# Kernel optimization log

Measured on AMD Instinct MI355X. Metric: run time of the kernel, lower is better.

## Reference

```python
import jax, jax.numpy as jnp
import numpy as np

NEG = jnp.float32(-1e30)  # finite stand-in for -inf in masked max
SLOPE = 0.01              # F.leaky_relu default negative slope


def _lrelu(v):
    return jnp.where(v >= 0, v, SLOPE * v)


def _mlp(pts, w1, b1, w2, b2, w3, b3):
    # pts: [2, N] -> [64, N]; 1x1 Conv1d == pointwise linear over channel dim
    z = _lrelu(w1 @ pts + b1[:, None])
    z = _lrelu(w2 @ z + b2[:, None])
    z = _lrelu(w3 @ z + b3[:, None])
    return z


def setup_inputs() -> dict:
    key = jax.random.key(0)
    ks = jax.random.split(key, 10)
    B, C, H, W = 4, 19, 256, 256
    x = jax.random.randint(ks[0], (B, C, H, W), 0, 2, dtype=jnp.int32)
    # grid exactly as in the torch module: meshgrid of two linspaces, flattened
    g = np.array(np.meshgrid(np.linspace(-1, 1, 256), np.linspace(-1, 1, 256),
                             sparse=False)).astype(np.float32)  # [2,256,256]
    grid = jnp.asarray(g.reshape(2, -1))  # [2, 65536]
    w1 = jax.random.normal(ks[1], (64, 2), jnp.float32) * 0.5
    b1 = jax.random.normal(ks[2], (64,), jnp.float32) * 0.1
    w2 = jax.random.normal(ks[3], (64, 64), jnp.float32) * 0.125
    b2 = jax.random.normal(ks[4], (64,), jnp.float32) * 0.1
    w3 = jax.random.normal(ks[5], (64, 64), jnp.float32) * 0.125
    b3 = jax.random.normal(ks[6], (64,), jnp.float32) * 0.1
    fcw = jax.random.normal(ks[7], (512, 64 * C), jnp.float32)
    fcb = jax.random.normal(ks[8], (512,), jnp.float32) * 0.1
    return {"x": x, "grid": grid, "w1": w1, "b1": b1, "w2": w2, "b2": b2,
            "w3": w3, "b3": b3, "fcw": fcw, "fcb": fcb}


def reference(x, grid, w1, b1, w2, b2, w3, b3, fcw, fcb):
    B, C = x.shape[0], x.shape[1]
    # Pointwise MLP on the shared grid once (grid identical for all b,c)
    feats = _mlp(grid, w1, b1, w2, b2, w3, b3)                 # [64, N]
    # Fallback feature for empty masks: MLP on a single zero point
    zero_feat = _mlp(jnp.zeros((2, 1), feats.dtype),
                     w1, b1, w2, b2, w3, b3)[:, 0]             # [64]
    mask = (x.reshape(B, C, -1) == 1)                          # [B, C, N]
    # Masked max over the ragged point sets, fully vectorized
    masked = jnp.where(mask[:, :, None, :], feats[None, None], NEG)
    z = jnp.max(masked, axis=-1)                               # [B, C, 64]
    empty = ~jnp.any(mask, axis=-1)                            # [B, C]
    z = jnp.where(empty[..., None], zero_feat, z)
    flat = z.reshape(B, C * 64)                                # channel-major cat
    # EqualLinear: weight scaled by 1/sqrt(in_dim) (lr_mul=1)
    scale = jnp.float32(1.0 / np.sqrt(C * 64))
    out = flat @ (fcw * scale).T + fcb                         # [B, 512]
    return jnp.repeat(out[:, None, :], 18, axis=1)             # [B, 18, 512]
```

## Files before the change

### kernel.cpp

```cpp
#include <hip/hip_runtime.h>

#define NPTS  65536
#define NBC   76
#define NREP  8
#define KEYN  4864

typedef _Float16 f16;
typedef __fp16   h16x2 __attribute__((ext_vector_type(2)));
typedef _Float16 f16x8 __attribute__((ext_vector_type(8)));
typedef float    f32x4 __attribute__((ext_vector_type(4)));

__device__ __forceinline__ float lrelu(float v) { return fmaxf(v, 0.01f * v); }

__device__ __forceinline__ unsigned pkrtz(float lo, float hi) {
  h16x2 p = __builtin_amdgcn_cvt_pkrtz(lo, hi);
  return __builtin_bit_cast(unsigned, p);
}
__device__ __forceinline__ unsigned pkey(unsigned u) {
  unsigned t = (u >> 15) & 0x00010001u;
  return u ^ (0x80008000u | (t * 0x7FFFu));
}
__device__ __forceinline__ unsigned pkmax(unsigned a, unsigned b) {
  unsigned d;
  asm("v_pk_max_u16 %0, %1, %2" : "=v"(d) : "v"(a), "v"(b));
  return d;
}
__device__ __forceinline__ unsigned sext1(unsigned x, int b) {
  return (unsigned)(((int)(x << (31 - b))) >> 31);
}

__device__ __forceinline__ void mfma_layer(
    const f16* __restrict__ A, const f16* __restrict__ B,
    const float* __restrict__ bias,
    int chb, int c15, int q, int pt0, int pt1,
    f32x4& acc0, f32x4& acc1)
{
  float4 bv = *(const float4*)(bias + chb + q * 4);
  acc0 = (f32x4){bv.x, bv.y, bv.z, bv.w};
  acc1 = acc0;
  #pragma unroll
  for (int k0 = 0; k0 < 64; k0 += 32) {
    f16x8 af = *(const f16x8*)&A[(chb + c15) * 72 + k0 + q * 8];
    f16x8 b0 = *(const f16x8*)&B[pt0 * 72 + k0 + q * 8];
    f16x8 b1 = *(const f16x8*)&B[pt1 * 72 + k0 + q * 8];
    acc0 = __builtin_amdgcn_mfma_f32_16x16x32_f16(af, b0, acc0, 0, 0, 0);
    acc1 = __builtin_amdgcn_mfma_f32_16x16x32_f16(af, b1, acc1, 0, 0, 0);
  }
}

__device__ __forceinline__ void layer1(
    f16* __restrict__ zA, const float* __restrict__ w1,
    const float* __restrict__ b1, int wv, int lane, float g0, float g1)
{
  unsigned uo[4];
  #pragma unroll
  for (int p = 0; p < 4; ++p) {
    int j = wv * 8 + p * 2;
    float z0 = lrelu(w1[2 * j] * g0 + w1[2 * j + 1] * g1 + b1[j]);
    float z1 = lrelu(w1[2 * j + 2] * g0 + w1[2 * j + 3] * g1 + b1[j + 1]);
    uo[p] = pkrtz(z0, z1);
  }
  *(uint4*)&zA[lane * 72 + wv * 8] = make_uint4(uo[0], uo[1], uo[2], uo[3]);
}

__global__ __launch_bounds__(512, 4) void kA_mlp(
    const float* __restrict__ grid,
    const float* __restrict__ w1, const float* __restrict__ b1,
    const float* __restrict__ w2, const float* __restrict__ b2,
    const float* __restrict__ w3, const float* __restrict__ b3,
    unsigned* __restrict__ kbuf)
{
  __shared__ __align__(16) unsigned char smem[55296];
  f16* zA0 = (f16*)(smem);
  f16* zA1 = (f16*)(smem + 9216);
  f16* zB0 = (f16*)(smem + 18432);
  f16* zB1 = (f16*)(smem + 27648);
  f16* wf2 = (f16*)(smem + 36864);
  f16* wf3 = (f16*)(smem + 46080);

  const int t = threadIdx.x, lane = t & 63, wv = t >> 6;
  const int n0 = blockIdx.x * 128;

  float g0a = grid[n0 + lane],      g1a = grid[NPTS + n0 + lane];
  float g0b = grid[n0 + 64 + lane], g1b = grid[NPTS + n0 + 64 + lane];

  {
    int ch = t >> 3, k0 = (t & 7) * 8;
    const float4* s2 = (const float4*)(w2 + ch * 64 + k0);
    float4 a = s2[0], b = s2[1];
    *(uint4*)&wf2[ch * 72 + k0] =
        make_uint4(pkrtz(a.x, a.y), pkrtz(a.z, a.w), pkrtz(b.x, b.y), pkrtz(b.z, b.w));
    const float4* s3 = (const float4*)(w3 + ch * 64 + k0);
    float4 c = s3[0], d = s3[1];
    *(uint4*)&wf3[ch * 72 + k0] =
        make_uint4(pkrtz(c.x, c.y), pkrtz(c.z, c.w), pkrtz(d.x, d.y), pkrtz(d.z, d.w));
  }
  layer1(zA0, w1, b1, wv, lane, g0a, g1a);
  __syncthreads();

  const int chb = (wv & 3) * 16, pth = (wv >> 2) * 32;
  const int c15 = lane & 15, q = lane >> 4;
  const int chq = chb + q * 4;
  const int pt0 = pth + c15, pt1 = pth + 16 + c15;
  const int r0 = chq >> 1;

  {
    f32x4 a0, a1;
    mfma_layer(wf2, zA0, b2, chb, c15, q, pt0, pt1, a0, a1);
    *(uint2*)&zB0[pt0 * 72 + chq] =
        make_uint2(pkrtz(lrelu(a0[0]), lrelu(a0[1])), pkrtz(lrelu(a0[2]), lrelu(a0[3])));
    *(uint2*)&zB0[pt1 * 72 + chq] =
        make_uint2(pkrtz(lrelu(a1[0]), lrelu(a1[1])), pkrtz(lrelu(a1[2]), lrelu(a1[3])));
  }
  layer1(zA1, w1, b1, wv, lane, g0b, g1b);
  __syncthreads();

  {
    f32x4 c0, c1;
    mfma_layer(wf3, zB0, b3, chb, c15, q, pt0, pt1, c0, c1);
    unsigned* kb = kbuf + (unsigned)(blockIdx.x * 2) * 2048;
    kb[r0 * 64 + pt0]       = pkey(pkrtz(lrelu(c0[0]), lrelu(c0[1])));
    kb[(r0 + 1) * 64 + pt0] = pkey(pkrtz(lrelu(c0[2]), lrelu(c0[3])));
    kb[r0 * 64 + pt1]       = pkey(pkrtz(lrelu(c1[0]), lrelu(c1[1])));
    kb[(r0 + 1) * 64 + pt1] = pkey(pkrtz(lrelu(c1[2]), lrelu(c1[3])));
  }
  {
    f32x4 a0, a1;
    mfma_layer(wf2, zA1, b2, chb, c15, q, pt0, pt1, a0, a1);
    *(uint2*)&zB1[pt0 * 72 + chq] =
        make_uint2(pkrtz(lrelu(a0[0]), lrelu(a0[1])), pkrtz(lrelu(a0[2]), lrelu(a0[3])));
    *(uint2*)&zB1[pt1 * 72 + chq] =
        make_uint2(pkrtz(lrelu(a1[0]), lrelu(a1[1])), pkrtz(lrelu(a1[2]), lrelu(a1[3])));
  }
  __syncthreads();

  {
    f32x4 c0, c1;
    mfma_layer(wf3, zB1, b3, chb, c15, q, pt0, pt1, c0, c1);
    unsigned* kb = kbuf + (unsigned)(blockIdx.x * 2 + 1) * 2048;
    kb[r0 * 64 + pt0]       = pkey(pkrtz(lrelu(c0[0]), lrelu(c0[1])));
    kb[(r0 + 1) * 64 + pt0] = pkey(pkrtz(lrelu(c0[2]), lrelu(c0[3])));
    kb[r0 * 64 + pt1]       = pkey(pkrtz(lrelu(c1[0]), lrelu(c1[1])));
    kb[(r0 + 1) * 64 + pt1] = pkey(pkrtz(lrelu(c1[2]), lrelu(c1[3])));
  }
}

__device__ __forceinline__ void phaseB(
    const unsigned* __restrict__ zk, const unsigned* mlo, const unsigned* mhi,
    unsigned* uacc, int rw)
{
  #pragma unroll
  for (int np = 0; np < 16; ++np) {
    uint4 z4 = *(const uint4*)&zk[rw * 68 + np * 4];
    const int p = np * 4, pb = p & 31;
    #pragma unroll
    for (int ii = 0; ii < 5; ++ii) {
      unsigned m = (p < 32) ? mlo[ii] : mhi[ii];
      unsigned s0 = sext1(m, pb),     s1 = sext1(m, pb + 1);
      unsigned s2 = sext1(m, pb + 2), s3 = sext1(m, pb + 3);
      unsigned a = uacc[ii];
      a = pkmax(a, z4.x & s0); a = pkmax(a, z4.y & s1);
      a = pkmax(a, z4.z & s2); a = pkmax(a, z4.w & s3);
      uacc[ii] = a;
    }
  }
}

__global__ __launch_bounds__(512, 8) void kB_max(
    const int* __restrict__ x, const unsigned* __restrict__ kbuf,
    unsigned* __restrict__ keys)
{
  __shared__ unsigned zk0[32 * 68], zk1[32 * 68];
  __shared__ unsigned long long mb0[NBC], mb1[NBC];

  const int t = threadIdx.x, lane = t & 63, wv = t >> 6;
  const int n0 = blockIdx.x * 128;

  uint4 kv0 = *(const uint4*)(kbuf + (unsigned)(blockIdx.x * 2) * 2048 + t * 4);
  uint4 kv1 = *(const uint4*)(kbuf + (unsigned)(blockIdx.x * 2 + 1) * 2048 + t * 4);

  *(uint4*)&zk0[(t >> 4) * 68 + (t & 15) * 4] = kv0;

  {
    int xa[10];
    #pragma unroll
    for (int i = 0; i < 10; ++i) {
      int bc = wv + 8 * i;
      if (bc < NBC) xa[i] = x[(bc << 16) + n0 + lane];
    }
    #pragma unroll
    for (int i = 0; i < 10; ++i) {
      int bc = wv + 8 * i;
      if (bc < NBC) {
        unsigned long long m = __ballot(xa[i] == 1);
        if (lane == 0) mb0[bc] = m;
      }
    }
    #pragma unroll
    for (int i = 0; i < 10; ++i) {
      int bc = wv + 8 * i;
      if (bc < NBC) xa[i] = x[(bc << 16) + n0 + 64 + lane];
    }
    #pragma unroll
    for (int i = 0; i < 10; ++i) {
      int bc = wv + 8 * i;
      if (bc < NBC) {
        unsigned long long m = __ballot(xa[i] == 1);
        if (lane == 0) mb1[bc] = m;
      }
    }
  }
  __syncthreads();
  *(uint4*)&zk1[(t >> 4) * 68 + (t & 15) * 4] = kv1;

  const int rw = t & 31, bg = t >> 5;
  const int bc0 = bg * 5;

  unsigned uacc[5] = {0u, 0u, 0u, 0u, 0u};
  unsigned mlo[5], mhi[5];

  #pragma unroll
  for (int ii = 0; ii < 5; ++ii) {
    int bc = bc0 + ii;
    unsigned long long m = (bc < NBC) ? mb0[bc] : 0ull;
    mlo[ii] = (unsigned)m; mhi[ii] = (unsigned)(m >> 32);
  }
  phaseB(zk0, mlo, mhi, uacc, rw);
  __syncthreads();
  #pragma unroll
  for (int ii = 0; ii < 5; ++ii) {
    int bc = bc0 + ii;
    unsigned long long m = (bc < NBC) ? mb1[bc] : 0ull;
    mlo[ii] = (unsigned)m; mhi[ii] = (unsigned)(m >> 32);
  }
  phaseB(zk1, mlo, mhi, uacc, rw);

  unsigned* krep = keys + (blockIdx.x & (NREP - 1)) * KEYN;
  #pragma unroll
  for (int ii = 0; ii < 5; ++ii) {
    int bc = bc0 + ii;
    if (bc < NBC) {
      unsigned lo = uacc[ii] & 0xFFFFu, hi = uacc[ii] >> 16;
      if (lo) atomicMax(&krep[bc * 64 + 2 * rw], lo);
      if (hi) atomicMax(&krep[bc * 64 + 2 * rw + 1], hi);
    }
  }
}

__global__ __launch_bounds__(256) void k2_fc(
    const unsigned* __restrict__ keys,
    const float* __restrict__ b1, const float* __restrict__ w2,
    const float* __restrict__ b2, const float* __restrict__ w3,
    const float* __restrict__ b3,
    const float* __restrict__ fcw, const float* __restrict__ fcb,
    float* __restrict__ out)
{
  __shared__ float flat[4864];
  __shared__ float za[64], zb[64], zf[64];
  const int t = threadIdx.x;

  if (t < 64) za[t] = lrelu(b1[t]);
  __syncthreads();
  if (t < 64) {
    float s = b2[t];
    #pragma unroll 8
    for (int k = 0; k < 64; ++k) s += w2[t * 64 + k] * za[k];
    zb[t] = lrelu(s);
  }
  __syncthreads();
  if (t < 64) {
    float s = b3[t];
    #pragma unroll 8
    for (int k = 0; k < 64; ++k) s += w3[t * 64 + k] * zb[k];
    zf[t] = lrelu(s);
  }
  __syncthreads();

  for (int idx = t; idx < 4864; idx += 256) {
    unsigned m = keys[idx];
    #pragma unroll
    for (int r = 1; r < NREP; ++r) m = max(m, keys[r * KEYN + idx]);
    float v;
    if (m) {
      unsigned u = (m & 0x8000u) ? (m ^ 0x8000u) : (~m & 0xFFFFu);
      unsigned short us = (unsigned short)u;
      v = (float)__builtin_bit_cast(f16, us);
    } else {
      v = zf[idx & 63];
    }
    flat[idx] = v;
  }
  __syncthreads();

  const int wv = t >> 6, lane = t & 63;
  const int o = blockIdx.x * 4 + wv;
  const float* wrow = fcw + o * 1216;
  float fa0 = 0.f, fa1 = 0.f, fa2 = 0.f, fa3 = 0.f;
  #pragma unroll
  for (int i = 0; i < 19; ++i) {
    int jj = i * 64 + lane;
    float wvv = wrow[jj];
    fa0 += wvv * flat[jj];
    fa1 += wvv * flat[1216 + jj];
    fa2 += wvv * flat[2432 + jj];
    fa3 += wvv * flat[3648 + jj];
  }
  #pragma unroll
  for (int off = 32; off > 0; off >>= 1) {
    fa0 += __shfl_xor(fa0, off);
    fa1 += __shfl_xor(fa1, off);
    fa2 += __shfl_xor(fa2, off);
    fa3 += __shfl_xor(fa3, off);
  }
  const float scale = 0.028676966733820225f;
  float cb = fcb[o];
  if (lane < 18) {
    out[(0 * 18 + lane) * 512 + o] = fa0 * scale + cb;
    out[(1 * 18 + lane) * 512 + o] = fa1 * scale + cb;
    out[(2 * 18 + lane) * 512 + o] = fa2 * scale + cb;
    out[(3 * 18 + lane) * 512 + o] = fa3 * scale + cb;
  }
}

extern "C" void kernel_launch(void* const* d_in, const int* in_sizes, int n_in,
                              void* d_out, int out_size, void* d_ws, size_t ws_size,
                              hipStream_t stream)
{
  const int*   x    = (const int*)d_in[0];
  const float* grid = (const float*)d_in[1];
  const float* w1   = (const float*)d_in[2];
  const float* b1   = (const float*)d_in[3];
  const float* w2   = (const float*)d_in[4];
  const float* b2   = (const float*)d_in[5];
  const float* w3   = (const float*)d_in[6];
  const float* b3   = (const float*)d_in[7];
  const float* fcw  = (const float*)d_in[8];
  const float* fcb  = (const float*)d_in[9];
  float* out = (float*)d_out;

  unsigned* keys = (unsigned*)d_ws;
  unsigned* kbuf = (unsigned*)d_ws + 65536;

  (void)hipMemsetAsync(d_ws, 0, NREP * KEYN * sizeof(unsigned), stream);
  hipLaunchKernelGGL(kA_mlp, dim3(512), dim3(512), 0, stream,
                     grid, w1, b1, w2, b2, w3, b3, kbuf);
  hipLaunchKernelGGL(kB_max, dim3(512), dim3(512), 0, stream,
                     x, kbuf, keys);
  hipLaunchKernelGGL(k2_fc, dim3(128), dim3(256), 0, stream,
                     keys, b1, w2, b2, w3, b3, fcw, fcb, out);
}
```

Baseline: 126.7 us.

## Fold key zeroing into MLP kernel and keep fp16 weights in registers

Removes the separate hipMemsetAsync by having the first 76 blocks of the MLP kernel zero the key buffer (76*512 = NREP*KEYN entries). Layer-2/3 weight fragments are now loaded from global and converted straight into registers instead of staged in shared memory, which cuts LDS use from 55 KB to 36 KB. Launch bounds are raised to 8 blocks per CU, and the layer-1 and layer-2 work is reordered so both point halves run between fewer barriers. The cost is redundant per-wave global weight loads and more register pressure under the tighter occupancy bound.

```diff
diff --git a/kernel.cpp b/kernel.cpp
--- a/kernel.cpp
+++ b/kernel.cpp
@@ -28,23 +28,27 @@
 __device__ __forceinline__ unsigned sext1(unsigned x, int b) {
   return (unsigned)(((int)(x << (31 - b))) >> 31);
 }
-
-__device__ __forceinline__ void mfma_layer(
-    const f16* __restrict__ A, const f16* __restrict__ B,
-    const float* __restrict__ bias,
-    int chb, int c15, int q, int pt0, int pt1,
-    f32x4& acc0, f32x4& acc1)
-{
-  float4 bv = *(const float4*)(bias + chb + q * 4);
+__device__ __forceinline__ f16x8 ldcvt8(const float* p) {
+  float4 a = *(const float4*)p, b = *(const float4*)(p + 4);
+  uint4 u = make_uint4(pkrtz(a.x, a.y), pkrtz(a.z, a.w),
+                       pkrtz(b.x, b.y), pkrtz(b.z, b.w));
+  return __builtin_bit_cast(f16x8, u);
+}
+
+__device__ __forceinline__ void mfma_layer_r(
+    const f16x8* wr, const f16* __restrict__ B, const float* __restrict__ bias,
+    int chq, int q, int pt0, int pt1, f32x4& acc0, f32x4& acc1)
+{
+  float4 bv = *(const float4*)(bias + chq);
   acc0 = (f32x4){bv.x, bv.y, bv.z, bv.w};
   acc1 = acc0;
   #pragma unroll
-  for (int k0 = 0; k0 < 64; k0 += 32) {
-    f16x8 af = *(const f16x8*)&A[(chb + c15) * 72 + k0 + q * 8];
+  for (int s = 0; s < 2; ++s) {
+    int k0 = s * 32;
     f16x8 b0 = *(const f16x8*)&B[pt0 * 72 + k0 + q * 8];
     f16x8 b1 = *(const f16x8*)&B[pt1 * 72 + k0 + q * 8];
-    acc0 = __builtin_amdgcn_mfma_f32_16x16x32_f16(af, b0, acc0, 0, 0, 0);
-    acc1 = __builtin_amdgcn_mfma_f32_16x16x32_f16(af, b1, acc1, 0, 0, 0);
+    acc0 = __builtin_amdgcn_mfma_f32_16x16x32_f16(wr[s], b0, acc0, 0, 0, 0);
+    acc1 = __builtin_amdgcn_mfma_f32_16x16x32_f16(wr[s], b1, acc1, 0, 0, 0);
   }
 }
 
@@ -63,40 +67,26 @@
   *(uint4*)&zA[lane * 72 + wv * 8] = make_uint4(uo[0], uo[1], uo[2], uo[3]);
 }
 
-__global__ __launch_bounds__(512, 4) void kA_mlp(
+__global__ __launch_bounds__(512, 8) void kA_mlp(
     const float* __restrict__ grid,
     const float* __restrict__ w1, const float* __restrict__ b1,
     const float* __restrict__ w2, const float* __restrict__ b2,
     const float* __restrict__ w3, const float* __restrict__ b3,
-    unsigned* __restrict__ kbuf)
-{
-  __shared__ __align__(16) unsigned char smem[55296];
+    unsigned* __restrict__ kbuf, unsigned* __restrict__ keys)
+{
+  __shared__ __align__(16) unsigned char smem[36864];
   f16* zA0 = (f16*)(smem);
   f16* zA1 = (f16*)(smem + 9216);
   f16* zB0 = (f16*)(smem + 18432);
   f16* zB1 = (f16*)(smem + 27648);
-  f16* wf2 = (f16*)(smem + 36864);
-  f16* wf3 = (f16*)(smem + 46080);
 
   const int t = threadIdx.x, lane = t & 63, wv = t >> 6;
   const int n0 = blockIdx.x * 128;
 
+  if (blockIdx.x < 76) keys[blockIdx.x * 512 + t] = 0u;
+
   float g0a = grid[n0 + lane],      g1a = grid[NPTS + n0 + lane];
   float g0b = grid[n0 + 64 + lane], g1b = grid[NPTS + n0 + 64 + lane];
-
-  {
-    int ch = t >> 3, k0 = (t & 7) * 8;
-    const float4* s2 = (const float4*)(w2 + ch * 64 + k0);
-    float4 a = s2[0], b = s2[1];
-    *(uint4*)&wf2[ch * 72 + k0] =
-        make_uint4(pkrtz(a.x, a.y), pkrtz(a.z, a.w), pkrtz(b.x, b.y), pkrtz(b.z, b.w));
-    const float4* s3 = (const float4*)(w3 + ch * 64 + k0);
-    float4 c = s3[0], d = s3[1];
-    *(uint4*)&wf3[ch * 72 + k0] =
-        make_uint4(pkrtz(c.x, c.y), pkrtz(c.z, c.w), pkrtz(d.x, d.y), pkrtz(d.z, d.w));
-  }
-  layer1(zA0, w1, b1, wv, lane, g0a, g1a);
-  __syncthreads();
 
   const int chb = (wv & 3) * 16, pth = (wv >> 2) * 32;
   const int c15 = lane & 15, q = lane >> 4;
@@ -104,44 +94,45 @@
   const int pt0 = pth + c15, pt1 = pth + 16 + c15;
   const int r0 = chq >> 1;
 
+  f16x8 wr2[2], wr3[2];
   {
-    f32x4 a0, a1;
-    mfma_layer(wf2, zA0, b2, chb, c15, q, pt0, pt1, a0, a1);
-    *(uint2*)&zB0[pt0 * 72 + chq] =
-        make_uint2(pkrtz(lrelu(a0[0]), lrelu(a0[1])), pkrtz(lrelu(a0[2]), lrelu(a0[3])));
-    *(uint2*)&zB0[pt1 * 72 + chq] =
-        make_uint2(pkrtz(lrelu(a1[0]), lrelu(a1[1])), pkrtz(lrelu(a1[2]), lrelu(a1[3])));
-  }
+    const int row = (chb + c15) * 64 + q * 8;
+    wr2[0] = ldcvt8(w2 + row);  wr2[1] = ldcvt8(w2 + row + 32);
+    wr3[0] = ldcvt8(w3 + row);  wr3[1] = ldcvt8(w3 + row + 32);
+  }
+
+  layer1(zA0, w1, b1, wv, lane, g0a, g1a);
   layer1(zA1, w1, b1, wv, lane, g0b, g1b);
   __syncthreads();
 
+  f32x4 a0, a1;
+  mfma_layer_r(wr2, zA0, b2, chq, q, pt0, pt1, a0, a1);
+  *(uint2*)&zB0[pt0 * 72 + chq] =
+      make_uint2(pkrtz(lrelu(a0[0]), lrelu(a0[1])), pkrtz(lrelu(a0[2]), lrelu(a0[3])));
+  *(uint2*)&zB0[pt1 * 72 + chq] =
+      make_uint2(pkrtz(lrelu(a1[0]), lrelu(a1[1])), pkrtz(lrelu(a1[2]), lrelu(a1[3])));
+  mfma_layer_r(wr2, zA1, b2, chq, q, pt0, pt1, a0, a1);
+  *(uint2*)&zB1[pt0 * 72 + chq] =
+      make_uint2(pkrtz(lrelu(a0[0]), lrelu(a0[1])), pkrtz(lrelu(a0[2]), lrelu(a0[3])));
+  *(uint2*)&zB1[pt1 * 72 + chq] =
+      make_uint2(pkrtz(lrelu(a1[0]), lrelu(a1[1])), pkrtz(lrelu(a1[2]), lrelu(a1[3])));
+  __syncthreads();
+
+  mfma_layer_r(wr3, zB0, b3, chq, q, pt0, pt1, a0, a1);
   {
-    f32x4 c0, c1;
-    mfma_layer(wf3, zB0, b3, chb, c15, q, pt0, pt1, c0, c1);
     unsigned* kb = kbuf + (unsigned)(blockIdx.x * 2) * 2048;
-    kb[r0 * 64 + pt0]       = pkey(pkrtz(lrelu(c0[0]), lrelu(c0[1])));
-    kb[(r0 + 1) * 64 + pt0] = pkey(pkrtz(lrelu(c0[2]), lrelu(c0[3])));
-    kb[r0 * 64 + pt1]       = pkey(pkrtz(lrelu(c1[0]), lrelu(c1[1])));
-    kb[(r0 + 1) * 64 + pt1] = pkey(pkrtz(lrelu(c1[2]), lrelu(c1[3])));
-  }
+    kb[r0 * 64 + pt0]       = pkey(pkrtz(lrelu(a0[0]), lrelu(a0[1])));
+    kb[(r0 + 1) * 64 + pt0] = pkey(pkrtz(lrelu(a0[2]), lrelu(a0[3])));
+    kb[r0 * 64 + pt1]       = pkey(pkrtz(lrelu(a1[0]), lrelu(a1[1])));
+    kb[(r0 + 1) * 64 + pt1] = pkey(pkrtz(lrelu(a1[2]), lrelu(a1[3])));
+  }
+  mfma_layer_r(wr3, zB1, b3, chq, q, pt0, pt1, a0, a1);
   {
-    f32x4 a0, a1;
-    mfma_layer(wf2, zA1, b2, chb, c15, q, pt0, pt1, a0, a1);
-    *(uint2*)&zB1[pt0 * 72 + chq] =
-        make_uint2(pkrtz(lrelu(a0[0]), lrelu(a0[1])), pkrtz(lrelu(a0[2]), lrelu(a0[3])));
-    *(uint2*)&zB1[pt1 * 72 + chq] =
-        make_uint2(pkrtz(lrelu(a1[0]), lrelu(a1[1])), pkrtz(lrelu(a1[2]), lrelu(a1[3])));
-  }
-  __syncthreads();
-
-  {
-    f32x4 c0, c1;
-    mfma_layer(wf3, zB1, b3, chb, c15, q, pt0, pt1, c0, c1);
     unsigned* kb = kbuf + (unsigned)(blockIdx.x * 2 + 1) * 2048;
-    kb[r0 * 64 + pt0]       = pkey(pkrtz(lrelu(c0[0]), lrelu(c0[1])));
-    kb[(r0 + 1) * 64 + pt0] = pkey(pkrtz(lrelu(c0[2]), lrelu(c0[3])));
-    kb[r0 * 64 + pt1]       = pkey(pkrtz(lrelu(c1[0]), lrelu(c1[1])));
-    kb[(r0 + 1) * 64 + pt1] = pkey(pkrtz(lrelu(c1[2]), lrelu(c1[3])));
+    kb[r0 * 64 + pt0]       = pkey(pkrtz(lrelu(a0[0]), lrelu(a0[1])));
+    kb[(r0 + 1) * 64 + pt0] = pkey(pkrtz(lrelu(a0[2]), lrelu(a0[3])));
+    kb[r0 * 64 + pt1]       = pkey(pkrtz(lrelu(a1[0]), lrelu(a1[1])));
+    kb[(r0 + 1) * 64 + pt1] = pkey(pkrtz(lrelu(a1[2]), lrelu(a1[3])));
   }
 }
 
@@ -178,7 +169,6 @@
 
   uint4 kv0 = *(const uint4*)(kbuf + (unsigned)(blockIdx.x * 2) * 2048 + t * 4);
   uint4 kv1 = *(const uint4*)(kbuf + (unsigned)(blockIdx.x * 2 + 1) * 2048 + t * 4);
-
   *(uint4*)&zk0[(t >> 4) * 68 + (t & 15) * 4] = kv0;
 
   {
@@ -218,7 +208,6 @@
 
   unsigned uacc[5] = {0u, 0u, 0u, 0u, 0u};
   unsigned mlo[5], mhi[5];
-
   #pragma unroll
   for (int ii = 0; ii < 5; ++ii) {
     int bc = bc0 + ii;
@@ -341,9 +330,8 @@
   unsigned* keys = (unsigned*)d_ws;
   unsigned* kbuf = (unsigned*)d_ws + 65536;
 
-  (void)hipMemsetAsync(d_ws, 0, NREP * KEYN * sizeof(unsigned), stream);
   hipLaunchKernelGGL(kA_mlp, dim3(512), dim3(512), 0, stream,
-                     grid, w1, b1, w2, b2, w3, b3, kbuf);
+                     grid, w1, b1, w2, b2, w3, b3, kbuf, keys);
   hipLaunchKernelGGL(kB_max, dim3(512), dim3(512), 0, stream,
                      x, kbuf, keys);
   hipLaunchKernelGGL(k2_fc, dim3(128), dim3(256), 0, stream,
```

Result: no change. 125.0 us (-1.3%).
